# Performance work log

Hardware: AMD Instinct MI355X
Metric: run time of the kernel (lower is better)

## Reference

```python
import jax, jax.numpy as jnp
import numpy as np

QUANT_BLOCK = 32  # GGUF Q4_0-style block size
QUANT_ZERO = 8.0  # 4-bit codes are offset-binary around 8


def setup_inputs() -> dict:
    key = jax.random.key(0)
    k_x, k_q, k_s, k_up, k_dn, k_b = jax.random.split(key, 6)
    O, I, R = 4096, 4096, 16
    T = 2048  # tokens (batch*seq)
    x = jax.random.normal(k_x, (T, I), dtype=jnp.float32)
    # quantized 4-bit codes stored unpacked as int32 in [0, 16)
    q = jax.random.randint(k_q, (O, I), 0, 16, dtype=jnp.int32)
    # per-block scales (small positive, like real GGUF d values)
    scales = jax.random.uniform(k_s, (O, I // QUANT_BLOCK), dtype=jnp.float32) * 0.05
    lora_up = jax.random.normal(k_up, (O, R), dtype=jnp.float32) * 0.02
    lora_down = jax.random.normal(k_dn, (R, I), dtype=jnp.float32) * 0.02
    alpha = jnp.ones((), dtype=jnp.float32)
    bias = jax.random.normal(k_b, (O,), dtype=jnp.float32)
    return {"x": x, "q": q, "scales": scales, "lora_up": lora_up,
            "lora_down": lora_down, "alpha": alpha, "bias": bias}


def _dequant(q, scales):
    # q: [O, I] int codes; scales: [O, I/BLOCK] per-block scale
    O, I = q.shape
    qf = q.reshape(O, I // QUANT_BLOCK, QUANT_BLOCK).astype(scales.dtype)
    w = (qf - QUANT_ZERO) * scales[:, :, None]  # [O, I/B, B]
    return w.reshape(O, I)


def reference(x, q, scales, lora_up, lora_down, alpha, bias):
    # on-the-fly dequant (GGMLLayer.get_weight -> dequantize_tensor)
    W = _dequant(q, scales)  # [O, I]
    # LoRA patch apply (ray_calculate_weight): W += alpha * up @ down
    W = W + alpha * jnp.einsum('or,ri->oi', lora_up, lora_down)
    # linear forward: y = x @ W^T + b
    return jnp.einsum('ti,oi->to', x, W) + bias
```

## Files before the change

### kernel.cpp

```cpp
#include <hip/hip_runtime.h>
#include <hip/hip_bf16.h>
#include <stdint.h>

#define T_DIM 2048
#define I_DIM 4096
#define O_DIM 4096
#define R_DIM 16
#define QBLK  32

typedef __bf16 bf16x8 __attribute__((ext_vector_type(8)));
typedef float  floatx4 __attribute__((ext_vector_type(4)));
typedef unsigned short ushort_t;

#define AS1 __attribute__((address_space(1)))
#define AS3 __attribute__((address_space(3)))

__device__ __forceinline__ ushort_t f2bf(float f) {
  unsigned u = __float_as_uint(f);
  u += 0x7FFFu + ((u >> 16) & 1u);
  return (ushort_t)(u >> 16);
}

__device__ __forceinline__ float dot4(float4 a, float4 b) {
  return a.x * b.x + a.y * b.y + a.z * b.z + a.w * b.w;
}

__global__ __launch_bounds__(256) void k_stream(const float* __restrict__ x,
                                                const int* __restrict__ q,
                                                const float* __restrict__ scales,
                                                ushort_t* __restrict__ xb,
                                                ushort_t* __restrict__ wb) {
  const int b = blockIdx.x, tid = threadIdx.x;
  if (b < 512) {
    const int stride = 512 * 256;
    const int u0 = b * 256 + tid;
    float4 v[4][4];
#pragma unroll
    for (int j = 0; j < 4; ++j) {
      const float4* p = (const float4*)x + (size_t)(u0 + j * stride) * 4;
      v[j][0] = p[0]; v[j][1] = p[1]; v[j][2] = p[2]; v[j][3] = p[3];
    }
#pragma unroll
    for (int j = 0; j < 4; ++j) {
      const size_t u = u0 + (size_t)j * stride;
      union { ushort_t us[16]; uint4 o[2]; } r;
#pragma unroll
      for (int k = 0; k < 4; ++k) {
        r.us[k * 4 + 0] = f2bf(v[j][k].x); r.us[k * 4 + 1] = f2bf(v[j][k].y);
        r.us[k * 4 + 2] = f2bf(v[j][k].z); r.us[k * 4 + 3] = f2bf(v[j][k].w);
      }
      ((uint4*)xb)[u * 2] = r.o[0];
      ((uint4*)xb)[u * 2 + 1] = r.o[1];
    }
    return;
  }
  {
    const int stride = 1024 * 256;
    const int u0 = (b - 512) * 256 + tid;
    int4 v[4][4];
    float s[4];
#pragma unroll
    for (int j = 0; j < 4; ++j) {
      const size_t u = u0 + (size_t)j * stride;
      const int4* p = (const int4*)q + u * 4;
      v[j][0] = p[0]; v[j][1] = p[1]; v[j][2] = p[2]; v[j][3] = p[3];
      const size_t e = u * 16;
      s[j] = scales[(e >> 12) * (I_DIM / QBLK) + ((e & 4095) >> 5)];
    }
#pragma unroll
    for (int j = 0; j < 4; ++j) {
      const size_t u = u0 + (size_t)j * stride;
      const float sj = s[j];
      union { ushort_t us[16]; uint4 o[2]; } r;
#pragma unroll
      for (int k = 0; k < 4; ++k) {
        r.us[k * 4 + 0] = f2bf((float)(v[j][k].x - 8) * sj);
        r.us[k * 4 + 1] = f2bf((float)(v[j][k].y - 8) * sj);
        r.us[k * 4 + 2] = f2bf((float)(v[j][k].z - 8) * sj);
        r.us[k * 4 + 3] = f2bf((float)(v[j][k].w - 8) * sj);
      }
      ((uint4*)wb)[u * 2] = r.o[0];
      ((uint4*)wb)[u * 2 + 1] = r.o[1];
    }
  }
}

__global__ __launch_bounds__(256) void k_xd(const float* __restrict__ x,
                                            const float* __restrict__ down,
                                            const float* __restrict__ alphap,
                                            float* __restrict__ xd) {
  __shared__ float ds[16 * 512];
  const int b = blockIdx.x, tid = threadIdx.x;
  const int tl = tid >> 5, s = tid & 31;
  const int t = b * 8 + tl;
  float acc[16];
#pragma unroll
  for (int r = 0; r < 16; ++r) acc[r] = 0.f;
  for (int c = 0; c < 8; ++c) {
    const int ib = c * 512;
    __syncthreads();
#pragma unroll
    for (int j = 0; j < 8; ++j) {
      int e = j * 256 + tid;
      int r = e >> 7, col = e & 127;
      ((float4*)ds)[e] = ((const float4*)(down + (size_t)r * I_DIM + ib))[col];
    }
    __syncthreads();
#pragma unroll
    for (int j = 0; j < 4; ++j) {
      float4 xv = ((const float4*)(x + (size_t)t * I_DIM + ib))[s + 32 * j];
#pragma unroll
      for (int r = 0; r < 16; ++r) {
        float4 dv = ((const float4*)ds)[r * 128 + s + 32 * j];
        acc[r] += dot4(xv, dv);
      }
    }
  }
  const float al = alphap[0];
#pragma unroll
  for (int r = 0; r < 16; ++r) {
    float v = acc[r];
    v += __shfl_down(v, 16, 32);
    v += __shfl_down(v, 8, 32);
    v += __shfl_down(v, 4, 32);
    v += __shfl_down(v, 2, 32);
    v += __shfl_down(v, 1, 32);
    if (s == 0) xd[t * 16 + r] = v * al;
  }
}


#define BK 64
#define NT (I_DIM / BK)
#define ASZ (128 * BK)
#define BSZ (256 * BK)

__device__ __forceinline__ bf16x8 lds_read16(unsigned addr) {
  bf16x8 d;
  asm volatile("ds_read_b128 %0, %1" : "=v"(d) : "v"(addr));
  return d;
}

__device__ __forceinline__ void stage6(const ushort_t* __restrict__ ga,
                                       const ushort_t* __restrict__ gb,
                                       ushort_t* Ast, ushort_t* Bst, int tid) {
#pragma unroll
  for (int it = 0; it < 2; ++it) {
    const int seg = it * 512 + tid;
    const int r = seg >> 3, cg = (seg & 7) ^ (r & 7);
    __builtin_amdgcn_global_load_lds(
        (const AS1 char*)(ga + (size_t)r * I_DIM + cg * 8),
        (AS3 char*)(Ast + (size_t)seg * 8), 16, 0, 0);
  }
#pragma unroll
  for (int it = 0; it < 4; ++it) {
    const int seg = it * 512 + tid;
    const int r = seg >> 3, cg = (seg & 7) ^ (r & 7);
    __builtin_amdgcn_global_load_lds(
        (const AS1 char*)(gb + (size_t)r * I_DIM + cg * 8),
        (AS3 char*)(Bst + (size_t)seg * 8), 16, 0, 0);
  }
}

template<int VM, bool STG>
__device__ __forceinline__ void ktile(unsigned aB, unsigned bB,
                                      ushort_t* Ast, ushort_t* Bst,
                                      const ushort_t* ga, const ushort_t* gb,
                                      floatx4 (&acc)[4][4], int tid) {
  const int lane = tid & 63, wv = tid >> 6;
  const int quad = lane >> 4, m16 = lane & 15;
  const int wm = wv >> 2, wn = wv & 3;

  if constexpr (STG) stage6(ga, gb, Ast, Bst, tid);

  bf16x8 a0[4], b0[4], a1[4], b1[4];
#pragma unroll
  for (int i = 0; i < 4; ++i) {
    const int m = wm * 64 + i * 16 + m16;
    a0[i] = lds_read16(aB + (unsigned)((m * 8 + (quad ^ (m & 7))) * 16));
  }
#pragma unroll
  for (int i = 0; i < 4; ++i) {
    const int n = wn * 64 + i * 16 + m16;
    b0[i] = lds_read16(bB + (unsigned)((n * 8 + (quad ^ (n & 7))) * 16));
  }
#pragma unroll
  for (int i = 0; i < 4; ++i) {
    const int m = wm * 64 + i * 16 + m16;
    a1[i] = lds_read16(aB + (unsigned)((m * 8 + ((4 + quad) ^ (m & 7))) * 16));
  }
#pragma unroll
  for (int i = 0; i < 4; ++i) {
    const int n = wn * 64 + i * 16 + m16;
    b1[i] = lds_read16(bB + (unsigned)((n * 8 + ((4 + quad) ^ (n & 7))) * 16));
  }
  asm volatile("s_waitcnt lgkmcnt(8)" ::: "memory");
  __builtin_amdgcn_sched_barrier(0);
  __builtin_amdgcn_s_setprio(1);
#pragma unroll
  for (int i = 0; i < 4; ++i)
#pragma unroll
    for (int j = 0; j < 4; ++j)
      acc[i][j] = __builtin_amdgcn_mfma_f32_16x16x32_bf16(a0[i], b0[j], acc[i][j], 0, 0, 0);
  __builtin_amdgcn_s_setprio(0);
  asm volatile("s_waitcnt lgkmcnt(0)" ::: "memory");
  __builtin_amdgcn_sched_barrier(0);
  __builtin_amdgcn_s_setprio(1);
#pragma unroll
  for (int i = 0; i < 4; ++i)
#pragma unroll
    for (int j = 0; j < 4; ++j)
      acc[i][j] = __builtin_amdgcn_mfma_f32_16x16x32_bf16(a1[i], b1[j], acc[i][j], 0, 0, 0);
  __builtin_amdgcn_s_setprio(0);
  if constexpr (VM == 6)      asm volatile("s_waitcnt vmcnt(6)" ::: "memory");
  else if constexpr (VM == 0) asm volatile("s_waitcnt vmcnt(0)" ::: "memory");
  if constexpr (VM >= 0) __builtin_amdgcn_sched_barrier(0);
  __builtin_amdgcn_s_barrier();
}

__global__ __launch_bounds__(512, 2) void k_gemm(const ushort_t* __restrict__ xb,
                                                 const ushort_t* __restrict__ wb,
                                                 const float* __restrict__ bias,
                                                 const float* __restrict__ xd,
                                                 const float* __restrict__ up,
                                                 float* __restrict__ y) {
  __shared__ __align__(16) ushort_t As[3][ASZ];
  __shared__ __align__(16) ushort_t Bs[3][BSZ];

  const int tid = threadIdx.x;

  const int id = blockIdx.x;
  const int xcd = id & 7, slot = id >> 3;
  const int bx = xcd * 2 + (slot & 1);
  const int by = slot >> 1;
  const int oT = bx * 256, tT = by * 128;

  const ushort_t* ap = xb + (size_t)tT * I_DIM;
  const ushort_t* bp = wb + (size_t)oT * I_DIM;

  const unsigned aL = (unsigned)(uintptr_t)(AS3 ushort_t*)&As[0][0];
  const unsigned bL = (unsigned)(uintptr_t)(AS3 ushort_t*)&Bs[0][0];
  const unsigned aS0 = aL, aS1 = aL + ASZ * 2, aS2 = aL + ASZ * 4;
  const unsigned bS0 = bL, bS1 = bL + BSZ * 2, bS2 = bL + BSZ * 4;

  floatx4 acc[4][4] = {};

  stage6(ap, bp, As[0], Bs[0], tid);
  stage6(ap + BK, bp + BK, As[1], Bs[1], tid);
  asm volatile("s_waitcnt vmcnt(6)" ::: "memory");
  __builtin_amdgcn_sched_barrier(0);
  __builtin_amdgcn_s_barrier();

  int kc = 2 * BK;
  for (int g = 0; g < 20; ++g) {
    ktile<6, true>(aS0, bS0, As[2], Bs[2], ap + kc, bp + kc, acc, tid); kc += BK;
    ktile<6, true>(aS1, bS1, As[0], Bs[0], ap + kc, bp + kc, acc, tid); kc += BK;
    ktile<6, true>(aS2, bS2, As[1], Bs[1], ap + kc, bp + kc, acc, tid); kc += BK;
  }
  ktile<6, true>(aS0, bS0, As[2], Bs[2], ap + kc, bp + kc, acc, tid); kc += BK;
  ktile<6, true>(aS1, bS1, As[0], Bs[0], ap + kc, bp + kc, acc, tid);
  ktile<0, false>(aS2, bS2, nullptr, nullptr, nullptr, nullptr, acc, tid);
  ktile<-1, false>(aS0, bS0, nullptr, nullptr, nullptr, nullptr, acc, tid);

  const int lane = tid & 63, wv = tid >> 6;
  const int quad = lane >> 4, m16 = lane & 15;
  const int wm = wv >> 2, wn = wv & 3;
#pragma unroll
  for (int im = 0; im < 4; ++im) {
#pragma unroll
    for (int reg = 0; reg < 4; ++reg) {
      const int t = tT + wm * 64 + im * 16 + quad * 4 + reg;
      const float4* xr = (const float4*)(xd + t * 16);
      float4 x0 = xr[0], x1 = xr[1], x2 = xr[2], x3 = xr[3];
#pragma unroll
      for (int in_ = 0; in_ < 4; ++in_) {
        const int o = oT + wn * 64 + in_ * 16 + m16;
        const float4* ur = (const float4*)(up + (size_t)o * R_DIM);
        float lv = dot4(x0, ur[0]) + dot4(x1, ur[1]) +
                   dot4(x2, ur[2]) + dot4(x3, ur[3]);
        y[(size_t)t * O_DIM + o] = acc[im][in_][reg] + lv + bias[o];
      }
    }
  }
}

extern "C" void kernel_launch(void* const* d_in, const int* in_sizes, int n_in,
                              void* d_out, int out_size, void* d_ws, size_t ws_size,
                              hipStream_t stream) {
  const float* x      = (const float*)d_in[0];
  const int*   q      = (const int*)d_in[1];
  const float* scales = (const float*)d_in[2];
  const float* up     = (const float*)d_in[3];
  const float* down   = (const float*)d_in[4];
  const float* alpha  = (const float*)d_in[5];
  const float* bias   = (const float*)d_in[6];
  float* y = (float*)d_out;

  ushort_t* xb = (ushort_t*)d_ws;
  ushort_t* wb = (ushort_t*)((char*)d_ws + (size_t)T_DIM * I_DIM * 2);
  float*    xd = (float*)((char*)d_ws + (size_t)T_DIM * I_DIM * 2 + (size_t)O_DIM * I_DIM * 2);

  hipLaunchKernelGGL(k_xd, dim3(256), dim3(256), 0, stream, x, down, alpha, xd);
  hipLaunchKernelGGL(k_stream, dim3(1536), dim3(256), 0, stream,
                     x, q, scales, xb, wb);
  hipLaunchKernelGGL(k_gemm, dim3((O_DIM / 256) * (T_DIM / 128)), dim3(512), 0, stream,
                     xb, wb, bias, xd, up, y);
}
```

Before: 426.5 us.

## Enlarge GEMM tile to 256x256 with double-buffered, phase-interleaved half-tile staging

```diff
diff --git a/kernel.cpp b/kernel.cpp
--- a/kernel.cpp
+++ b/kernel.cpp
@@ -132,8 +132,8 @@
 
 #define BK 64
 #define NT (I_DIM / BK)
-#define ASZ (128 * BK)
-#define BSZ (256 * BK)
+#define SLOT_E (256 * BK)
+#define HALF_E (128 * BK)
 
 __device__ __forceinline__ bf16x8 lds_read16(unsigned addr) {
   bf16x8 d;
@@ -141,78 +141,105 @@
   return d;
 }
 
-__device__ __forceinline__ void stage6(const ushort_t* __restrict__ ga,
-                                       const ushort_t* __restrict__ gb,
-                                       ushort_t* Ast, ushort_t* Bst, int tid) {
+__device__ __forceinline__ void stage_half(const ushort_t* __restrict__ g,
+                                           ushort_t* dst, int tid) {
 #pragma unroll
   for (int it = 0; it < 2; ++it) {
     const int seg = it * 512 + tid;
     const int r = seg >> 3, cg = (seg & 7) ^ (r & 7);
     __builtin_amdgcn_global_load_lds(
-        (const AS1 char*)(ga + (size_t)r * I_DIM + cg * 8),
-        (AS3 char*)(Ast + (size_t)seg * 8), 16, 0, 0);
-  }
-#pragma unroll
-  for (int it = 0; it < 4; ++it) {
-    const int seg = it * 512 + tid;
-    const int r = seg >> 3, cg = (seg & 7) ^ (r & 7);
-    __builtin_amdgcn_global_load_lds(
-        (const AS1 char*)(gb + (size_t)r * I_DIM + cg * 8),
-        (AS3 char*)(Bst + (size_t)seg * 8), 16, 0, 0);
-  }
-}
-
-template<int VM, bool STG>
+        (const AS1 char*)(g + (size_t)r * I_DIM + cg * 8),
+        (AS3 char*)(dst + (size_t)seg * 8), 16, 0, 0);
+  }
+}
+
+#define PHASE_SYNC()                                          \
+  __builtin_amdgcn_s_barrier();                               \
+  asm volatile("s_waitcnt lgkmcnt(0)" ::: "memory");          \
+  __builtin_amdgcn_sched_barrier(0);                          \
+  __builtin_amdgcn_s_setprio(1)
+
+#define PHASE_END()                                           \
+  __builtin_amdgcn_s_setprio(0);                              \
+  __builtin_amdgcn_s_barrier()
+
+template<int VM, bool SA, bool SB_>
 __device__ __forceinline__ void ktile(unsigned aB, unsigned bB,
                                       ushort_t* Ast, ushort_t* Bst,
-                                      const ushort_t* ga, const ushort_t* gb,
-                                      floatx4 (&acc)[4][4], int tid) {
-  const int lane = tid & 63, wv = tid >> 6;
-  const int quad = lane >> 4, m16 = lane & 15;
-  const int wm = wv >> 2, wn = wv & 3;
-
-  if constexpr (STG) stage6(ga, gb, Ast, Bst, tid);
-
-  bf16x8 a0[4], b0[4], a1[4], b1[4];
+                                      const ushort_t* gA, const ushort_t* gB,
+                                      floatx4 (&acc)[8][4],
+                                      int wm, int wn, int quad, int m16, int tid) {
+  bf16x8 a0[4], a1[4], b0k0[2], b0k1[2], b1k0[2], b1k1[2];
+
 #pragma unroll
   for (int i = 0; i < 4; ++i) {
-    const int m = wm * 64 + i * 16 + m16;
+    const int m = wm * 128 + i * 16 + m16;
     a0[i] = lds_read16(aB + (unsigned)((m * 8 + (quad ^ (m & 7))) * 16));
-  }
+    a1[i] = lds_read16(aB + (unsigned)((m * 8 + ((4 + quad) ^ (m & 7))) * 16));
+  }
+#pragma unroll
+  for (int j = 0; j < 2; ++j) {
+    const int n = wn * 64 + j * 16 + m16;
+    b0k0[j] = lds_read16(bB + (unsigned)((n * 8 + (quad ^ (n & 7))) * 16));
+    b0k1[j] = lds_read16(bB + (unsigned)((n * 8 + ((4 + quad) ^ (n & 7))) * 16));
+  }
+  if constexpr (SA) stage_half(gA, Ast, tid);
+  PHASE_SYNC();
+#pragma unroll
+  for (int i = 0; i < 4; ++i)
+#pragma unroll
+    for (int j = 0; j < 2; ++j) {
+      acc[i][j] = __builtin_amdgcn_mfma_f32_16x16x32_bf16(a0[i], b0k0[j], acc[i][j], 0, 0, 0);
+      acc[i][j] = __builtin_amdgcn_mfma_f32_16x16x32_bf16(a1[i], b0k1[j], acc[i][j], 0, 0, 0);
+    }
+  PHASE_END();
+
+#pragma unroll
+  for (int j = 0; j < 2; ++j) {
+    const int n = wn * 64 + (2 + j) * 16 + m16;
+    b1k0[j] = lds_read16(bB + (unsigned)((n * 8 + (quad ^ (n & 7))) * 16));
+    b1k1[j] = lds_read16(bB + (unsigned)((n * 8 + ((4 + quad) ^ (n & 7))) * 16));
+  }
+  if constexpr (SA) stage_half(gA + (size_t)128 * I_DIM, Ast + HALF_E, tid);
+  PHASE_SYNC();
+#pragma unroll
+  for (int i = 0; i < 4; ++i)
+#pragma unroll
+    for (int j = 0; j < 2; ++j) {
+      acc[i][2 + j] = __builtin_amdgcn_mfma_f32_16x16x32_bf16(a0[i], b1k0[j], acc[i][2 + j], 0, 0, 0);
+      acc[i][2 + j] = __builtin_amdgcn_mfma_f32_16x16x32_bf16(a1[i], b1k1[j], acc[i][2 + j], 0, 0, 0);
+    }
+  PHASE_END();
+
 #pragma unroll
   for (int i = 0; i < 4; ++i) {
-    const int n = wn * 64 + i * 16 + m16;
-    b0[i] = lds_read16(bB + (unsigned)((n * 8 + (quad ^ (n & 7))) * 16));
-  }
-#pragma unroll
-  for (int i = 0; i < 4; ++i) {
-    const int m = wm * 64 + i * 16 + m16;
+    const int m = wm * 128 + 64 + i * 16 + m16;
+    a0[i] = lds_read16(aB + (unsigned)((m * 8 + (quad ^ (m & 7))) * 16));
     a1[i] = lds_read16(aB + (unsigned)((m * 8 + ((4 + quad) ^ (m & 7))) * 16));
   }
-#pragma unroll
-  for (int i = 0; i < 4; ++i) {
-    const int n = wn * 64 + i * 16 + m16;
-    b1[i] = lds_read16(bB + (unsigned)((n * 8 + ((4 + quad) ^ (n & 7))) * 16));
-  }
-  asm volatile("s_waitcnt lgkmcnt(8)" ::: "memory");
-  __builtin_amdgcn_sched_barrier(0);
+  if constexpr (SB_) stage_half(gB, Bst, tid);
+  PHASE_SYNC();
+#pragma unroll
+  for (int i = 0; i < 4; ++i)
+#pragma unroll
+    for (int j = 0; j < 2; ++j) {
+      acc[4 + i][j] = __builtin_amdgcn_mfma_f32_16x16x32_bf16(a0[i], b0k0[j], acc[4 + i][j], 0, 0, 0);
+      acc[4 + i][j] = __builtin_amdgcn_mfma_f32_16x16x32_bf16(a1[i], b0k1[j], acc[4 + i][j], 0, 0, 0);
+    }
+  PHASE_END();
+
+  if constexpr (SB_) stage_half(gB + (size_t)128 * I_DIM, Bst + HALF_E, tid);
+  __builtin_amdgcn_s_barrier();
   __builtin_amdgcn_s_setprio(1);
 #pragma unroll
   for (int i = 0; i < 4; ++i)
 #pragma unroll
-    for (int j = 0; j < 4; ++j)
-      acc[i][j] = __builtin_amdgcn_mfma_f32_16x16x32_bf16(a0[i], b0[j], acc[i][j], 0, 0, 0);
+    for (int j = 0; j < 2; ++j) {
+      acc[4 + i][2 + j] = __builtin_amdgcn_mfma_f32_16x16x32_bf16(a0[i], b1k0[j], acc[4 + i][2 + j], 0, 0, 0);
+      acc[4 + i][2 + j] = __builtin_amdgcn_mfma_f32_16x16x32_bf16(a1[i], b1k1[j], acc[4 + i][2 + j], 0, 0, 0);
+    }
   __builtin_amdgcn_s_setprio(0);
-  asm volatile("s_waitcnt lgkmcnt(0)" ::: "memory");
-  __builtin_amdgcn_sched_barrier(0);
-  __builtin_amdgcn_s_setprio(1);
-#pragma unroll
-  for (int i = 0; i < 4; ++i)
-#pragma unroll
-    for (int j = 0; j < 4; ++j)
-      acc[i][j] = __builtin_amdgcn_mfma_f32_16x16x32_bf16(a1[i], b1[j], acc[i][j], 0, 0, 0);
-  __builtin_amdgcn_s_setprio(0);
-  if constexpr (VM == 6)      asm volatile("s_waitcnt vmcnt(6)" ::: "memory");
+  if constexpr (VM == 4)      asm volatile("s_waitcnt vmcnt(4)" ::: "memory");
   else if constexpr (VM == 0) asm volatile("s_waitcnt vmcnt(0)" ::: "memory");
   if constexpr (VM >= 0) __builtin_amdgcn_sched_barrier(0);
   __builtin_amdgcn_s_barrier();
@@ -224,61 +251,64 @@
                                                  const float* __restrict__ xd,
                                                  const float* __restrict__ up,
                                                  float* __restrict__ y) {
-  __shared__ __align__(16) ushort_t As[3][ASZ];
-  __shared__ __align__(16) ushort_t Bs[3][BSZ];
+  __shared__ __align__(16) ushort_t As[2][SLOT_E];
+  __shared__ __align__(16) ushort_t Bs[2][SLOT_E];
 
   const int tid = threadIdx.x;
-
-  const int id = blockIdx.x;
-  const int xcd = id & 7, slot = id >> 3;
-  const int bx = xcd * 2 + (slot & 1);
-  const int by = slot >> 1;
-  const int oT = bx * 256, tT = by * 128;
-
-  const ushort_t* ap = xb + (size_t)tT * I_DIM;
-  const ushort_t* bp = wb + (size_t)oT * I_DIM;
-
-  const unsigned aL = (unsigned)(uintptr_t)(AS3 ushort_t*)&As[0][0];
-  const unsigned bL = (unsigned)(uintptr_t)(AS3 ushort_t*)&Bs[0][0];
-  const unsigned aS0 = aL, aS1 = aL + ASZ * 2, aS2 = aL + ASZ * 4;
-  const unsigned bS0 = bL, bS1 = bL + BSZ * 2, bS2 = bL + BSZ * 4;
-
-  floatx4 acc[4][4] = {};
-
-  stage6(ap, bp, As[0], Bs[0], tid);
-  stage6(ap + BK, bp + BK, As[1], Bs[1], tid);
-  asm volatile("s_waitcnt vmcnt(6)" ::: "memory");
-  __builtin_amdgcn_sched_barrier(0);
-  __builtin_amdgcn_s_barrier();
-
-  int kc = 2 * BK;
-  for (int g = 0; g < 20; ++g) {
-    ktile<6, true>(aS0, bS0, As[2], Bs[2], ap + kc, bp + kc, acc, tid); kc += BK;
-    ktile<6, true>(aS1, bS1, As[0], Bs[0], ap + kc, bp + kc, acc, tid); kc += BK;
-    ktile<6, true>(aS2, bS2, As[1], Bs[1], ap + kc, bp + kc, acc, tid); kc += BK;
-  }
-  ktile<6, true>(aS0, bS0, As[2], Bs[2], ap + kc, bp + kc, acc, tid); kc += BK;
-  ktile<6, true>(aS1, bS1, As[0], Bs[0], ap + kc, bp + kc, acc, tid);
-  ktile<0, false>(aS2, bS2, nullptr, nullptr, nullptr, nullptr, acc, tid);
-  ktile<-1, false>(aS0, bS0, nullptr, nullptr, nullptr, nullptr, acc, tid);
-
   const int lane = tid & 63, wv = tid >> 6;
   const int quad = lane >> 4, m16 = lane & 15;
   const int wm = wv >> 2, wn = wv & 3;
-#pragma unroll
-  for (int im = 0; im < 4; ++im) {
+
+  const int oT = blockIdx.x * 256, tT = blockIdx.y * 256;
+  const ushort_t* ap = xb + (size_t)tT * I_DIM;
+  const ushort_t* bp = wb + (size_t)oT * I_DIM;
+
+  const unsigned aL = (unsigned)(uintptr_t)(AS3 ushort_t*)&As[0][0];
+  const unsigned bL = (unsigned)(uintptr_t)(AS3 ushort_t*)&Bs[0][0];
+  const unsigned A0 = aL, A1 = aL + SLOT_E * 2;
+  const unsigned B0 = bL, B1 = bL + SLOT_E * 2;
+
+  floatx4 acc[8][4] = {};
+
+  stage_half(ap, &As[0][0], tid);
+  stage_half(ap + (size_t)128 * I_DIM, &As[0][0] + HALF_E, tid);
+  stage_half(bp, &Bs[0][0], tid);
+  stage_half(bp + (size_t)128 * I_DIM, &Bs[0][0] + HALF_E, tid);
+  stage_half(bp + BK, &Bs[1][0], tid);
+  stage_half(bp + (size_t)128 * I_DIM + BK, &Bs[1][0] + HALF_E, tid);
+  asm volatile("s_waitcnt vmcnt(4)" ::: "memory");
+  __builtin_amdgcn_sched_barrier(0);
+  __builtin_amdgcn_s_barrier();
+
+  for (int g = 0; g < 31; ++g) {
+    const int kt = 2 * g;
+    ktile<4, true, true>(A0, B0, &As[1][0], &Bs[0][0],
+                         ap + (size_t)(kt + 1) * BK, bp + (size_t)(kt + 2) * BK,
+                         acc, wm, wn, quad, m16, tid);
+    ktile<4, true, true>(A1, B1, &As[0][0], &Bs[1][0],
+                         ap + (size_t)(kt + 2) * BK, bp + (size_t)(kt + 3) * BK,
+                         acc, wm, wn, quad, m16, tid);
+  }
+  ktile<0, true, false>(A0, B0, &As[1][0], nullptr,
+                        ap + (size_t)63 * BK, nullptr,
+                        acc, wm, wn, quad, m16, tid);
+  ktile<-1, false, false>(A1, B1, nullptr, nullptr, nullptr, nullptr,
+                          acc, wm, wn, quad, m16, tid);
+
+#pragma unroll
+  for (int im = 0; im < 8; ++im) {
 #pragma unroll
     for (int reg = 0; reg < 4; ++reg) {
-      const int t = tT + wm * 64 + im * 16 + quad * 4 + reg;
+      const int t = tT + wm * 128 + im * 16 + quad * 4 + reg;
       const float4* xr = (const float4*)(xd + t * 16);
       float4 x0 = xr[0], x1 = xr[1], x2 = xr[2], x3 = xr[3];
 #pragma unroll
-      for (int in_ = 0; in_ < 4; ++in_) {
-        const int o = oT + wn * 64 + in_ * 16 + m16;
+      for (int jn = 0; jn < 4; ++jn) {
+        const int o = oT + wn * 64 + jn * 16 + m16;
         const float4* ur = (const float4*)(up + (size_t)o * R_DIM);
         float lv = dot4(x0, ur[0]) + dot4(x1, ur[1]) +
                    dot4(x2, ur[2]) + dot4(x3, ur[3]);
-        y[(size_t)t * O_DIM + o] = acc[im][in_][reg] + lv + bias[o];
+        y[(size_t)t * O_DIM + o] = acc[im][jn][reg] + lv + bias[o];
       }
     }
   }
@@ -303,6 +333,6 @@
   hipLaunchKernelGGL(k_xd, dim3(256), dim3(256), 0, stream, x, down, alpha, xd);
   hipLaunchKernelGGL(k_stream, dim3(1536), dim3(256), 0, stream,
                      x, q, scales, xb, wb);
-  hipLaunchKernelGGL(k_gemm, dim3((O_DIM / 256) * (T_DIM / 128)), dim3(512), 0, stream,
+  hipLaunchKernelGGL(k_gemm, dim3(O_DIM / 256, T_DIM / 256), dim3(512), 0, stream,
                      xb, wb, bias, xd, up, y);
 }
```

Measured after the change: 706.6 us. 65.7% more time.

## Shrink GEMM tile to 128x64 with BK=32 and 256-thread blocks

Applied to the files above, without the earlier changes.

```diff
diff --git a/kernel.cpp b/kernel.cpp
--- a/kernel.cpp
+++ b/kernel.cpp
@@ -130,10 +130,10 @@
 }
 
 
-#define BK 64
+#define BK 32
 #define NT (I_DIM / BK)
-#define ASZ (128 * BK)
-#define BSZ (256 * BK)
+#define A_E (128 * BK)
+#define B_E (64 * BK)
 
 __device__ __forceinline__ bf16x8 lds_read16(unsigned addr) {
   bf16x8 d;
@@ -141,21 +141,20 @@
   return d;
 }
 
-__device__ __forceinline__ void stage6(const ushort_t* __restrict__ ga,
+__device__ __forceinline__ void stage3(const ushort_t* __restrict__ ga,
                                        const ushort_t* __restrict__ gb,
                                        ushort_t* Ast, ushort_t* Bst, int tid) {
 #pragma unroll
   for (int it = 0; it < 2; ++it) {
-    const int seg = it * 512 + tid;
-    const int r = seg >> 3, cg = (seg & 7) ^ (r & 7);
+    const int seg = it * 256 + tid;
+    const int r = seg >> 2, cg = (seg & 3) ^ (r & 3);
     __builtin_amdgcn_global_load_lds(
         (const AS1 char*)(ga + (size_t)r * I_DIM + cg * 8),
         (AS3 char*)(Ast + (size_t)seg * 8), 16, 0, 0);
   }
-#pragma unroll
-  for (int it = 0; it < 4; ++it) {
-    const int seg = it * 512 + tid;
-    const int r = seg >> 3, cg = (seg & 7) ^ (r & 7);
+  {
+    const int seg = tid;
+    const int r = seg >> 2, cg = (seg & 3) ^ (r & 3);
     __builtin_amdgcn_global_load_lds(
         (const AS1 char*)(gb + (size_t)r * I_DIM + cg * 8),
         (AS3 char*)(Bst + (size_t)seg * 8), 16, 0, 0);
@@ -166,105 +165,78 @@
 __device__ __forceinline__ void ktile(unsigned aB, unsigned bB,
                                       ushort_t* Ast, ushort_t* Bst,
                                       const ushort_t* ga, const ushort_t* gb,
-                                      floatx4 (&acc)[4][4], int tid) {
+                                      floatx4 (&acc)[4][2], int tid) {
   const int lane = tid & 63, wv = tid >> 6;
   const int quad = lane >> 4, m16 = lane & 15;
-  const int wm = wv >> 2, wn = wv & 3;
-
-  if constexpr (STG) stage6(ga, gb, Ast, Bst, tid);
-
-  bf16x8 a0[4], b0[4], a1[4], b1[4];
+  const int wm = wv >> 1, wn = wv & 1;
+
+  if constexpr (STG) stage3(ga, gb, Ast, Bst, tid);
+
+  bf16x8 af[4], bf[2];
 #pragma unroll
   for (int i = 0; i < 4; ++i) {
     const int m = wm * 64 + i * 16 + m16;
-    a0[i] = lds_read16(aB + (unsigned)((m * 8 + (quad ^ (m & 7))) * 16));
-  }
-#pragma unroll
-  for (int i = 0; i < 4; ++i) {
-    const int n = wn * 64 + i * 16 + m16;
-    b0[i] = lds_read16(bB + (unsigned)((n * 8 + (quad ^ (n & 7))) * 16));
-  }
-#pragma unroll
-  for (int i = 0; i < 4; ++i) {
-    const int m = wm * 64 + i * 16 + m16;
-    a1[i] = lds_read16(aB + (unsigned)((m * 8 + ((4 + quad) ^ (m & 7))) * 16));
-  }
-#pragma unroll
-  for (int i = 0; i < 4; ++i) {
-    const int n = wn * 64 + i * 16 + m16;
-    b1[i] = lds_read16(bB + (unsigned)((n * 8 + ((4 + quad) ^ (n & 7))) * 16));
-  }
-  asm volatile("s_waitcnt lgkmcnt(8)" ::: "memory");
-  __builtin_amdgcn_sched_barrier(0);
-  __builtin_amdgcn_s_setprio(1);
-#pragma unroll
-  for (int i = 0; i < 4; ++i)
-#pragma unroll
-    for (int j = 0; j < 4; ++j)
-      acc[i][j] = __builtin_amdgcn_mfma_f32_16x16x32_bf16(a0[i], b0[j], acc[i][j], 0, 0, 0);
-  __builtin_amdgcn_s_setprio(0);
+    af[i] = lds_read16(aB + (unsigned)((m * 4 + (quad ^ (m & 3))) * 16));
+  }
+#pragma unroll
+  for (int j = 0; j < 2; ++j) {
+    const int n = wn * 32 + j * 16 + m16;
+    bf[j] = lds_read16(bB + (unsigned)((n * 4 + (quad ^ (n & 3))) * 16));
+  }
   asm volatile("s_waitcnt lgkmcnt(0)" ::: "memory");
   __builtin_amdgcn_sched_barrier(0);
   __builtin_amdgcn_s_setprio(1);
 #pragma unroll
   for (int i = 0; i < 4; ++i)
 #pragma unroll
-    for (int j = 0; j < 4; ++j)
-      acc[i][j] = __builtin_amdgcn_mfma_f32_16x16x32_bf16(a1[i], b1[j], acc[i][j], 0, 0, 0);
+    for (int j = 0; j < 2; ++j)
+      acc[i][j] = __builtin_amdgcn_mfma_f32_16x16x32_bf16(af[i], bf[j], acc[i][j], 0, 0, 0);
   __builtin_amdgcn_s_setprio(0);
-  if constexpr (VM == 6)      asm volatile("s_waitcnt vmcnt(6)" ::: "memory");
+  if constexpr (VM == 3)      asm volatile("s_waitcnt vmcnt(3)" ::: "memory");
   else if constexpr (VM == 0) asm volatile("s_waitcnt vmcnt(0)" ::: "memory");
   if constexpr (VM >= 0) __builtin_amdgcn_sched_barrier(0);
   __builtin_amdgcn_s_barrier();
 }
 
-__global__ __launch_bounds__(512, 2) void k_gemm(const ushort_t* __restrict__ xb,
+__global__ __launch_bounds__(256, 4) void k_gemm(const ushort_t* __restrict__ xb,
                                                  const ushort_t* __restrict__ wb,
                                                  const float* __restrict__ bias,
                                                  const float* __restrict__ xd,
                                                  const float* __restrict__ up,
                                                  float* __restrict__ y) {
-  __shared__ __align__(16) ushort_t As[3][ASZ];
-  __shared__ __align__(16) ushort_t Bs[3][BSZ];
+  __shared__ __align__(16) ushort_t As[3][A_E];
+  __shared__ __align__(16) ushort_t Bs[3][B_E];
 
   const int tid = threadIdx.x;
-
-  const int id = blockIdx.x;
-  const int xcd = id & 7, slot = id >> 3;
-  const int bx = xcd * 2 + (slot & 1);
-  const int by = slot >> 1;
-  const int oT = bx * 256, tT = by * 128;
-
+  const int oT = blockIdx.x * 64, tT = blockIdx.y * 128;
   const ushort_t* ap = xb + (size_t)tT * I_DIM;
   const ushort_t* bp = wb + (size_t)oT * I_DIM;
 
   const unsigned aL = (unsigned)(uintptr_t)(AS3 ushort_t*)&As[0][0];
   const unsigned bL = (unsigned)(uintptr_t)(AS3 ushort_t*)&Bs[0][0];
-  const unsigned aS0 = aL, aS1 = aL + ASZ * 2, aS2 = aL + ASZ * 4;
-  const unsigned bS0 = bL, bS1 = bL + BSZ * 2, bS2 = bL + BSZ * 4;
-
-  floatx4 acc[4][4] = {};
-
-  stage6(ap, bp, As[0], Bs[0], tid);
-  stage6(ap + BK, bp + BK, As[1], Bs[1], tid);
-  asm volatile("s_waitcnt vmcnt(6)" ::: "memory");
+  const unsigned aS0 = aL, aS1 = aL + A_E * 2, aS2 = aL + A_E * 4;
+  const unsigned bS0 = bL, bS1 = bL + B_E * 2, bS2 = bL + B_E * 4;
+
+  floatx4 acc[4][2] = {};
+
+  stage3(ap, bp, As[0], Bs[0], tid);
+  stage3(ap + BK, bp + BK, As[1], Bs[1], tid);
+  asm volatile("s_waitcnt vmcnt(3)" ::: "memory");
   __builtin_amdgcn_sched_barrier(0);
   __builtin_amdgcn_s_barrier();
 
   int kc = 2 * BK;
-  for (int g = 0; g < 20; ++g) {
-    ktile<6, true>(aS0, bS0, As[2], Bs[2], ap + kc, bp + kc, acc, tid); kc += BK;
-    ktile<6, true>(aS1, bS1, As[0], Bs[0], ap + kc, bp + kc, acc, tid); kc += BK;
-    ktile<6, true>(aS2, bS2, As[1], Bs[1], ap + kc, bp + kc, acc, tid); kc += BK;
-  }
-  ktile<6, true>(aS0, bS0, As[2], Bs[2], ap + kc, bp + kc, acc, tid); kc += BK;
-  ktile<6, true>(aS1, bS1, As[0], Bs[0], ap + kc, bp + kc, acc, tid);
-  ktile<0, false>(aS2, bS2, nullptr, nullptr, nullptr, nullptr, acc, tid);
-  ktile<-1, false>(aS0, bS0, nullptr, nullptr, nullptr, nullptr, acc, tid);
+  for (int g = 0; g < 42; ++g) {
+    ktile<3, true>(aS0, bS0, As[2], Bs[2], ap + kc, bp + kc, acc, tid); kc += BK;
+    ktile<3, true>(aS1, bS1, As[0], Bs[0], ap + kc, bp + kc, acc, tid); kc += BK;
+    ktile<3, true>(aS2, bS2, As[1], Bs[1], ap + kc, bp + kc, acc, tid); kc += BK;
+  }
+  ktile<0, false>(aS0, bS0, nullptr, nullptr, nullptr, nullptr, acc, tid);
+  ktile<-1, false>(aS1, bS1, nullptr, nullptr, nullptr, nullptr, acc, tid);
 
   const int lane = tid & 63, wv = tid >> 6;
   const int quad = lane >> 4, m16 = lane & 15;
-  const int wm = wv >> 2, wn = wv & 3;
+  const int wm = wv >> 1, wn = wv & 1;
 #pragma unroll
   for (int im = 0; im < 4; ++im) {
 #pragma unroll
@@ -273,12 +245,12 @@
       const float4* xr = (const float4*)(xd + t * 16);
       float4 x0 = xr[0], x1 = xr[1], x2 = xr[2], x3 = xr[3];
 #pragma unroll
-      for (int in_ = 0; in_ < 4; ++in_) {
-        const int o = oT + wn * 64 + in_ * 16 + m16;
+      for (int jn = 0; jn < 2; ++jn) {
+        const int o = oT + wn * 32 + jn * 16 + m16;
         const float4* ur = (const float4*)(up + (size_t)o * R_DIM);
         float lv = dot4(x0, ur[0]) + dot4(x1, ur[1]) +
                    dot4(x2, ur[2]) + dot4(x3, ur[3]);
-        y[(size_t)t * O_DIM + o] = acc[im][in_][reg] + lv + bias[o];
+        y[(size_t)t * O_DIM + o] = acc[im][jn][reg] + lv + bias[o];
       }
     }
   }
@@ -303,6 +275,6 @@
   hipLaunchKernelGGL(k_xd, dim3(256), dim3(256), 0, stream, x, down, alpha, xd);
   hipLaunchKernelGGL(k_stream, dim3(1536), dim3(256), 0, stream,
                      x, q, scales, xb, wb);
-  hipLaunchKernelGGL(k_gemm, dim3((O_DIM / 256) * (T_DIM / 128)), dim3(512), 0, stream,
+  hipLaunchKernelGGL(k_gemm, dim3(O_DIM / 64, T_DIM / 128), dim3(256), 0, stream,
                      xb, wb, bias, xd, up, y);
 }
```

Result: slower. 455.7 us (+6.8%).
